# Performance work log

Hardware: AMD Instinct MI355X
Metric: run time of the kernel (lower is better)

The kernel has to match this reference:

```python
import jax, jax.numpy as jnp
import numpy as np

CAPACITY_FACTOR = 1.0


def setup_inputs() -> dict:
    key = jax.random.key(0)
    k = jax.random.split(key, 6)
    N, E, M, V = 8192, 8, 1024, 4096
    s = 0.02
    return {
        "x": jax.random.normal(k[0], (N, M), jnp.float32),
        "wg": jax.random.normal(k[1], (E, M), jnp.float32) * s,
        "fc1": jax.random.normal(k[2], (E, M, V), jnp.float32) * s,
        "b1": jax.random.normal(k[3], (E, V), jnp.float32) * s,
        "fc2": jax.random.normal(k[4], (E, V, M), jnp.float32) * s,
        "b2": jax.random.normal(k[5], (E, M), jnp.float32) * s,
    }


def reference(x, wg, fc1, b1, fc2, b2):
    N, M = x.shape
    E = wg.shape[0]
    capacity = 2 * int(CAPACITY_FACTOR * ((N + E - 1) // E))  # Top2 capacity

    # ---- Top2 gating ----
    logits = x @ wg.T                                   # [N, E]
    gates = jax.nn.softmax(logits, axis=1)
    _, top2 = jax.lax.top_k(logits, 2)                  # [N, 2]
    i1, i2 = top2[:, 0], top2[:, 1]
    m1 = jax.nn.one_hot(i1, E, dtype=jnp.int32)         # [N, E]
    m2 = jax.nn.one_hot(i2, E, dtype=jnp.int32)
    g1 = jnp.sum(gates * m1, axis=1)                    # [N]
    g2 = jnp.sum(gates * m2, axis=1)

    # cumulative-sum capacity assignment (per expert slot index)
    loc1 = jnp.cumsum(m1, axis=0) - 1                   # [N, E]
    loc2 = jnp.cumsum(m2, axis=0) - 1 + jnp.sum(m1, axis=0, keepdims=True)
    m1c = m1 * (loc1 < capacity).astype(jnp.int32)
    m2c = m2 * (loc2 < capacity).astype(jnp.int32)
    loc1_s = jnp.sum(loc1 * m1c, axis=1)                # [N]
    loc2_s = jnp.sum(loc2 * m2c, axis=1)
    v1 = jnp.sum(m1c, axis=1)                           # 0/1 kept flags
    v2 = jnp.sum(m2c, axis=1)

    # aux load-balancing loss (fp32 branch of original)
    me = jnp.sum(gates, axis=0)
    ce = jnp.sum(m1c.astype(gates.dtype), axis=0)
    l_aux = jnp.sum(me * ce) * (E / (N * N))

    # ---- dispatch (scatter tokens into [E*C, M]) ----
    idx1 = jnp.where(v1 > 0, i1 * capacity + loc1_s, -1)
    idx2 = jnp.where(v2 > 0, i2 * capacity + loc2_s, -1)
    disp = jnp.zeros((E * capacity, M), x.dtype)
    disp = disp.at[idx1].add(x, mode="drop")
    disp = disp.at[idx2].add(x, mode="drop")

    # ---- fused FFN experts ----
    d = disp.reshape(E, capacity, M)
    h = jnp.einsum("ecm,emv->ecv", d, fc1) + b1[:, None, :]
    h = jax.nn.relu(h)
    y = jnp.einsum("ecv,evm->ecm", h, fc2) + b2[:, None, :]
    yf = y.reshape(E * capacity, M)

    # ---- combine (gather + gate-weighted sum) ----
    v1f = v1.astype(x.dtype)
    v2f = v2.astype(x.dtype)
    out = (g1 * v1f)[:, None] * yf[i1 * capacity + loc1_s] \
        + (g2 * v2f)[:, None] * yf[i2 * capacity + loc2_s]
    return out, l_aux
```

## Files before the change

kernel.cpp:

```cpp
#include <hip/hip_runtime.h>
#include <stdint.h>

typedef __attribute__((ext_vector_type(8))) short short8;
typedef __attribute__((ext_vector_type(4))) float f32x4;

#define N_TOK 8192
#define E_EXP 8
#define M_DIM 1024
#define V_DIM 4096
#define CAP   2048
#define SLOTS (E_EXP*CAP)

__device__ __forceinline__ unsigned short f2bf(float f){
  unsigned u = __float_as_uint(f);
  u += 0x7FFFu + ((u >> 16) & 1u);
  return (unsigned short)(u >> 16);
}

__device__ __forceinline__ void gload_lds16(const void* g, void* l){
  __builtin_amdgcn_global_load_lds(
    (const __attribute__((address_space(1))) void*)g,
    (__attribute__((address_space(3))) void*)l, 16, 0, 0);
}

__global__ __launch_bounds__(256) void routing_kernel(
    const float* __restrict__ x, const float* __restrict__ wg,
    float* __restrict__ gates, int* __restrict__ i1o, int* __restrict__ i2o,
    float* __restrict__ g1o, float* __restrict__ g2o)
{
  int wv = threadIdx.x >> 6, lane = threadIdx.x & 63;
  int n = blockIdx.x * 4 + wv;
  const float* xr = x + (size_t)n * M_DIM;
  double acc[8];
  #pragma unroll
  for (int e = 0; e < 8; e++) acc[e] = 0.0;
  for (int j = 0; j < M_DIM/64; j++){
    double xv = (double)xr[lane + j*64];
    #pragma unroll
    for (int e = 0; e < 8; e++) acc[e] += xv * (double)wg[e*M_DIM + lane + j*64];
  }
  #pragma unroll
  for (int off = 32; off > 0; off >>= 1){
    #pragma unroll
    for (int e = 0; e < 8; e++) acc[e] += __shfl_down(acc[e], off);
  }
  if (lane == 0){
    float lg[8], mx = -1e30f;
    #pragma unroll
    for (int e = 0; e < 8; e++){ lg[e] = (float)acc[e]; mx = fmaxf(mx, lg[e]); }
    float s = 0.f, gt[8];
    #pragma unroll
    for (int e = 0; e < 8; e++){ gt[e] = expf(lg[e] - mx); s += gt[e]; }
    float inv = 1.f / s;
    int i1 = 0;
    #pragma unroll
    for (int e = 1; e < 8; e++) if (lg[e] > lg[i1]) i1 = e;
    int i2 = (i1 == 0) ? 1 : 0;
    #pragma unroll
    for (int e = 0; e < 8; e++){ if (e == i1) continue; if (lg[e] > lg[i2]) i2 = e; }
    #pragma unroll
    for (int e = 0; e < 8; e++) gates[(size_t)n*8 + e] = gt[e] * inv;
    i1o[n] = i1; i2o[n] = i2;
    g1o[n] = gt[i1] * inv; g2o[n] = gt[i2] * inv;
  }
}

__global__ __launch_bounds__(1024) void scan_kernel(
    const int* __restrict__ i1, const int* __restrict__ i2,
    int* __restrict__ s1, int* __restrict__ s2, int* __restrict__ ce_out)
{
  __shared__ unsigned long long sc[4][1024];
  const int t = threadIdx.x;
  int e1l[8], e2l[8];
  unsigned long long c[4] = {0ull,0ull,0ull,0ull};
  #pragma unroll
  for (int k = 0; k < 8; k++){
    int a = i1[t*8+k]; e1l[k] = a; c[a>>2]       += 1ull << ((a&3)*16);
    int b = i2[t*8+k]; e2l[k] = b; c[2 + (b>>2)] += 1ull << ((b&3)*16);
  }
  #pragma unroll
  for (int i = 0; i < 4; i++) sc[i][t] = c[i];
  __syncthreads();
  for (int st = 1; st < 1024; st <<= 1){
    unsigned long long add[4];
    #pragma unroll
    for (int i = 0; i < 4; i++) add[i] = (t >= st) ? sc[i][t-st] : 0ull;
    __syncthreads();
    #pragma unroll
    for (int i = 0; i < 4; i++) if (t >= st) sc[i][t] += add[i];
    __syncthreads();
  }
  unsigned long long ex[4], tot[4];
  #pragma unroll
  for (int i = 0; i < 4; i++){ ex[i] = sc[i][t] - c[i]; tot[i] = sc[i][1023]; }
  int r1[8], r2[8], t1[8];
  #pragma unroll
  for (int e = 0; e < 8; e++){
    r1[e] = (int)((ex[e>>2]       >> ((e&3)*16)) & 0xFFFF);
    r2[e] = (int)((ex[2 + (e>>2)] >> ((e&3)*16)) & 0xFFFF);
    t1[e] = (int)((tot[e>>2]      >> ((e&3)*16)) & 0xFFFF);
  }
  #pragma unroll
  for (int k = 0; k < 8; k++){
    int n = t*8 + k;
    int a = e1l[k]; int loc1 = r1[a]++;
    s1[n] = (loc1 < CAP) ? (a*CAP + loc1) : -1;
    int b = e2l[k]; int loc2 = r2[b]++ + t1[b];
    s2[n] = (loc2 < CAP) ? (b*CAP + loc2) : -1;
  }
  if (t == 0){
    #pragma unroll
    for (int e = 0; e < 8; e++) ce_out[e] = (t1[e] < CAP) ? t1[e] : CAP;
  }
}

__global__ __launch_bounds__(1024) void laux_kernel(
    const float* __restrict__ gates, const int* __restrict__ ce, float* __restrict__ dst)
{
  __shared__ float red[1024];
  const int t = threadIdx.x;
  float part[8];
  #pragma unroll
  for (int e = 0; e < 8; e++) part[e] = 0.f;
  for (int k = 0; k < 8; k++){
    int n = t + k*1024;
    #pragma unroll
    for (int e = 0; e < 8; e++) part[e] += gates[(size_t)n*8 + e];
  }
  float laux = 0.f;
  for (int e = 0; e < 8; e++){
    red[t] = part[e];
    __syncthreads();
    for (int s = 512; s > 0; s >>= 1){ if (t < s) red[t] += red[t+s]; __syncthreads(); }
    if (t == 0) laux += red[0] * (float)ce[e];
    __syncthreads();
  }
  if (t == 0) dst[0] = laux * (float)(8.0/(8192.0*8192.0));
}

__global__ void build_droplist(const int* __restrict__ s1, const int* __restrict__ s2,
                               int* __restrict__ list, int* __restrict__ cnt)
{
  int lane = threadIdx.x;
  int base = 0;
  int a = s1[lane], b = s2[lane];
  for (int it = 0; it < N_TOK/64; it++){
    int na = 0, nb = 0;
    if (it + 1 < N_TOK/64){
      na = s1[(it+1)*64 + lane];
      nb = s2[(it+1)*64 + lane];
    }
    int n = it*64 + lane;
    bool f1 = (a == -1) || (a == SLOTS-1);
    unsigned long long m1 = __ballot(f1);
    if (f1) list[base + __popcll(m1 & ((1ull<<lane)-1))] = n;
    base += __popcll(m1);
    bool f2 = (b == -1) || (b == SLOTS-1);
    unsigned long long m2 = __ballot(f2);
    if (f2) list[base + __popcll(m2 & ((1ull<<lane)-1))] = n;
    base += __popcll(m2);
    a = na; b = nb;
  }
  if (lane == 0) *cnt = base;
}

__global__ void dropacc1_kernel(const float* __restrict__ x, const int* __restrict__ list,
                                const int* __restrict__ cnt, float* __restrict__ partial)
{
  int col = blockIdx.x*256 + threadIdx.x;
  int sl  = blockIdx.y;
  int c = *cnt;
  int per = (c + 15) >> 4;
  int lo = sl*per, hi = lo + per; if (hi > c) hi = c;
  float a = 0.f;
  for (int i = lo; i < hi; i++) a += x[(size_t)list[i]*M_DIM + col];
  partial[sl*M_DIM + col] = a;
}
__global__ void dropacc2_kernel(const float* __restrict__ partial, float* __restrict__ drow)
{
  int col = blockIdx.x*256 + threadIdx.x;
  float s = 0.f;
  #pragma unroll
  for (int j = 0; j < 16; j++) s += partial[j*M_DIM + col];
  drow[col] = s;
}

template<bool RELU>
__global__ __launch_bounds__(256) void fix_gemv(
    const float* __restrict__ vec, const float* __restrict__ W,
    const float* __restrict__ bias, float* __restrict__ outv, int K, int N)
{
  __shared__ float red[256];
  const int o = threadIdx.x & 15;
  const int c = threadIdx.x >> 4;
  const int n = blockIdx.x*16 + o;
  const int chunk = K >> 4;
  float a = 0.f;
  for (int k = c*chunk; k < (c+1)*chunk; k++) a += vec[k] * W[(size_t)k*N + n];
  red[threadIdx.x] = a;
  __syncthreads();
  if (c == 0){
    float s = 0.f;
    #pragma unroll
    for (int j = 0; j < 16; j++) s += red[o + j*16];
    s += bias[n];
    if (RELU) s = fmaxf(s, 0.f);
    outv[n] = s;
  }
}

__global__ __launch_bounds__(256) void convert_x_kernel(
    const float* __restrict__ x, unsigned short* __restrict__ xb)
{
  size_t i = ((size_t)blockIdx.x*256 + threadIdx.x) * 8;
  float4 f0 = *(const float4*)(x + i);
  float4 f1 = *(const float4*)(x + i + 4);
  short8 v;
  v[0] = (short)f2bf(f0.x); v[1] = (short)f2bf(f0.y);
  v[2] = (short)f2bf(f0.z); v[3] = (short)f2bf(f0.w);
  v[4] = (short)f2bf(f1.x); v[5] = (short)f2bf(f1.y);
  v[6] = (short)f2bf(f1.z); v[7] = (short)f2bf(f1.w);
  *(short8*)(xb + i) = v;
}

__global__ void tok_fill_kernel(const int* __restrict__ s1, const int* __restrict__ s2,
                                int* __restrict__ tok)
{
  int n = blockIdx.x*256 + threadIdx.x;
  int a = s1[n], b = s2[n];
  if (a >= 0) tok[a] = n;
  if (b >= 0) tok[b] = n;
}

__global__ __launch_bounds__(256) void transpose_f32_bf16(
    const float* __restrict__ in, unsigned short* __restrict__ out,
    int R, int C, size_t estride)
{
  __shared__ float tile[32][33];
  const size_t eo = (size_t)blockIdx.z * estride;
  int c0 = blockIdx.x*32, r0 = blockIdx.y*32;
  int tx = threadIdx.x & 31, ty = threadIdx.x >> 5;
  #pragma unroll
  for (int j = 0; j < 4; j++)
    tile[ty + j*8][tx] = in[eo + (size_t)(r0 + ty + j*8)*C + (c0 + tx)];
  __syncthreads();
  #pragma unroll
  for (int j = 0; j < 4; j++)
    out[eo + (size_t)(c0 + ty + j*8)*R + (r0 + tx)] = f2bf(tile[tx][ty + j*8]);
}

template<bool RELU_BF16, bool AIND>
__global__ __launch_bounds__(512, 2) void gemm_tn(
    const unsigned short* __restrict__ A, size_t aE,
    const unsigned short* __restrict__ B, size_t bE,
    const float* __restrict__ bias, size_t biasE,
    void* __restrict__ outp, size_t oE, int K, int Ncols, int gx, int gy,
    const int* __restrict__ tok, const unsigned short* __restrict__ xb,
    const unsigned short* __restrict__ zrow, int slotbase)
{
  __shared__ unsigned short SH[65536];
  auto As = reinterpret_cast<unsigned short(*)[2][128*64]>(SH);
  auto Bs = reinterpret_cast<unsigned short(*)[2][128*64]>(SH + 32768);
  const int nwg = gridDim.x;
  const int orig = blockIdx.x;
  const int wgid = (orig & 7) * (nwg >> 3) + (orig >> 3);
  const int z  = wgid / (gx*gy);
  const int rr = wgid - z*gx*gy;
  const int by = rr / gx, bx = rr - by*gx;

  const unsigned short* Be = B + (size_t)z * bE;
  const float* be = bias + (size_t)z * biasE;
  const int row0 = by * 256;
  const int col0 = bx * 256;
  const int tid = threadIdx.x;
  const int lane = tid & 63, wv = tid >> 6;
  const int wr = wv >> 2, wc = wv & 3;
  const int frow = lane & 15, fq = lane >> 4;

  const int rbase = (wv*64 + lane) >> 3;
  const int swz   = (((lane & 7) ^ (rbase & 7)) * 8);
  const unsigned short* pA[2][2];
  const unsigned short* pB[2][2];
  #pragma unroll
  for (int h = 0; h < 2; h++)
    #pragma unroll
    for (int i = 0; i < 2; i++){
      int gr = row0 + h*128 + rbase + i*64;
      if (AIND){
        int tk = tok[slotbase + z*CAP + gr];
        pA[h][i] = (tk < 0) ? zrow : (xb + (size_t)tk * M_DIM);
      } else {
        pA[h][i] = A + (size_t)z * aE + (size_t)gr * K;
      }
      pB[h][i] = Be + (size_t)(col0 + h*128 + rbase + i*64) * K;
    }

  f32x4 acc[8][4];
  #pragma unroll
  for (int i = 0; i < 8; i++)
    #pragma unroll
    for (int j = 0; j < 4; j++) acc[i][j] = (f32x4){0.f,0.f,0.f,0.f};

  auto STAGE_A = [&](int buf, int half, int k0){
    #pragma unroll
    for (int i = 0; i < 2; i++)
      gload_lds16(pA[half][i] + k0 + swz, &As[buf][half][(i*512 + wv*64)*8]);
  };
  auto STAGE_B = [&](int buf, int half, int k0){
    #pragma unroll
    for (int i = 0; i < 2; i++)
      gload_lds16(pB[half][i] + k0 + swz, &Bs[buf][half][(i*512 + wv*64)*8]);
  };

  short8 a[8], bA[4], bB[4];
  auto READ_A = [&](int buf, int fmb){
    #pragma unroll
    for (int fm = 0; fm < 4; fm++)
      #pragma unroll
      for (int ks = 0; ks < 2; ks++){
        int row = wr*128 + (fmb+fm)*16 + frow;
        int h = row >> 7, r = row & 127;
        int sl = (ks*4 + fq) ^ (r & 7);
        a[fm*2+ks] = *(const short8*)&As[buf][h][r*64 + sl*8];
      }
  };
  auto READ_B = [&](int buf, int fnb, short8* dst){
    #pragma unroll
    for (int fn = 0; fn < 2; fn++)
      #pragma unroll
      for (int ks = 0; ks < 2; ks++){
        int col = wc*64 + (fnb+fn)*16 + frow;
        int h = col >> 7, r = col & 127;
        int sl = (ks*4 + fq) ^ (r & 7);
        dst[fn*2+ks] = *(const short8*)&Bs[buf][h][r*64 + sl*8];
      }
  };
  auto MFMA16 = [&](int fmb, int fnb, short8* b){
    #pragma unroll
    for (int fm = 0; fm < 4; fm++)
      #pragma unroll
      for (int fn = 0; fn < 2; fn++)
        #pragma unroll
        for (int ks = 0; ks < 2; ks++)
          acc[fmb+fm][fnb+fn] =
            __builtin_amdgcn_mfma_f32_16x16x32_bf16(a[fm*2+ks], b[fn*2+ks], acc[fmb+fm][fnb+fn], 0, 0, 0);
  };

  const int nt = K >> 6;
  const int iters = nt >> 1;
  STAGE_A(0, 0, 0); STAGE_A(0, 1, 0);
  STAGE_B(0, 0, 0); STAGE_B(0, 1, 0);
  STAGE_B(1, 0, 64); STAGE_B(1, 1, 64);
  asm volatile("s_waitcnt vmcnt(4)" ::: "memory");
  __builtin_amdgcn_sched_barrier(0);
  __builtin_amdgcn_s_barrier();

  for (int t = 0; t < iters; ++t){
    const bool more = (t + 1 < iters);
    const int kO = (2*t+1)*64;
    const int kN = (2*t+2)*64;
    const int kL = (2*t+3)*64;

    READ_A(0, 0); READ_B(0, 0, bA);
    STAGE_A(1, 0, kO);
    __builtin_amdgcn_s_barrier();
    asm volatile("s_waitcnt lgkmcnt(0)" ::: "memory");
    __builtin_amdgcn_sched_barrier(0);
    __builtin_amdgcn_s_setprio(1); MFMA16(0, 0, bA); __builtin_amdgcn_s_setprio(0);
    __builtin_amdgcn_s_barrier();
    READ_B(0, 2, bB);
    STAGE_A(1, 1, kO);
    __builtin_amdgcn_s_barrier();
    asm volatile("s_waitcnt lgkmcnt(0)" ::: "memory");
    __builtin_amdgcn_sched_barrier(0);
    __builtin_amdgcn_s_setprio(1); MFMA16(0, 2, bB); __builtin_amdgcn_s_setprio(0);
    __builtin_amdgcn_s_barrier();
    READ_A(0, 4);
    if (more) STAGE_B(0, 0, kN);
    __builtin_amdgcn_s_barrier();
    asm volatile("s_waitcnt lgkmcnt(0)" ::: "memory");
    __builtin_amdgcn_sched_barrier(0);
    __builtin_amdgcn_s_setprio(1); MFMA16(4, 0, bA); __builtin_amdgcn_s_setprio(0);
    __builtin_amdgcn_s_barrier();
    if (more) STAGE_B(0, 1, kN);
    __builtin_amdgcn_s_barrier();
    asm volatile("s_waitcnt lgkmcnt(0)" ::: "memory");
    __builtin_amdgcn_sched_barrier(0);
    __builtin_amdgcn_s_setprio(1); MFMA16(4, 2, bB); __builtin_amdgcn_s_setprio(0);
    if (more) asm volatile("s_waitcnt vmcnt(4)" ::: "memory");
    else      asm volatile("s_waitcnt vmcnt(0)" ::: "memory");
    __builtin_amdgcn_sched_barrier(0);
    __builtin_amdgcn_s_barrier();

    READ_A(1, 0); READ_B(1, 0, bA);
    if (more) STAGE_A(0, 0, kN);
    __builtin_amdgcn_s_barrier();
    asm volatile("s_waitcnt lgkmcnt(0)" ::: "memory");
    __builtin_amdgcn_sched_barrier(0);
    __builtin_amdgcn_s_setprio(1); MFMA16(0, 0, bA); __builtin_amdgcn_s_setprio(0);
    __builtin_amdgcn_s_barrier();
    READ_B(1, 2, bB);
    if (more) STAGE_A(0, 1, kN);
    __builtin_amdgcn_s_barrier();
    asm volatile("s_waitcnt lgkmcnt(0)" ::: "memory");
    __builtin_amdgcn_sched_barrier(0);
    __builtin_amdgcn_s_setprio(1); MFMA16(0, 2, bB); __builtin_amdgcn_s_setprio(0);
    __builtin_amdgcn_s_barrier();
    READ_A(1, 4);
    if (more) STAGE_B(1, 0, kL);
    __builtin_amdgcn_s_barrier();
    asm volatile("s_waitcnt lgkmcnt(0)" ::: "memory");
    __builtin_amdgcn_sched_barrier(0);
    __builtin_amdgcn_s_setprio(1); MFMA16(4, 0, bA); __builtin_amdgcn_s_setprio(0);
    __builtin_amdgcn_s_barrier();
    if (more) STAGE_B(1, 1, kL);
    __builtin_amdgcn_s_barrier();
    asm volatile("s_waitcnt lgkmcnt(0)" ::: "memory");
    __builtin_amdgcn_sched_barrier(0);
    __builtin_amdgcn_s_setprio(1); MFMA16(4, 2, bB); __builtin_amdgcn_s_setprio(0);
    if (more){
      asm volatile("s_waitcnt vmcnt(4)" ::: "memory");
      __builtin_amdgcn_sched_barrier(0);
    }
    __builtin_amdgcn_s_barrier();
  }

  const int rsub = fq * 4;
  if (RELU_BF16){
    unsigned short* ep = SH;
    #pragma unroll
    for (int fn = 0; fn < 4; fn++){
      int col = wc*64 + fn*16 + frow;
      float bv = be[col0 + col];
      #pragma unroll
      for (int fm = 0; fm < 8; fm++){
        int row = wr*128 + fm*16 + rsub;
        #pragma unroll
        for (int r = 0; r < 4; r++)
          ep[(row + r)*256 + col] = f2bf(fmaxf(acc[fm][fn][r] + bv, 0.f));
      }
    }
    __builtin_amdgcn_s_barrier();
    unsigned short* hp = (unsigned short*)outp + (size_t)z*oE;
    #pragma unroll
    for (int j = 0; j < 16; j++){
      int chunk = tid + j*512;
      int row = chunk >> 5, off = (chunk & 31)*8;
      *(short8*)(hp + (size_t)(row0 + row)*Ncols + col0 + off) = *(const short8*)&ep[row*256 + off];
    }
  } else {
    float* ep32 = (float*)SH;
    float* yp = (float*)outp + (size_t)z*oE;
    #pragma unroll
    for (int ph = 0; ph < 2; ph++){
      if (wr == ph){
        #pragma unroll
        for (int fn = 0; fn < 4; fn++){
          int col = wc*64 + fn*16 + frow;
          float bv = be[col0 + col];
          #pragma unroll
          for (int fm = 0; fm < 8; fm++){
            int rloc = fm*16 + rsub;
            #pragma unroll
            for (int r = 0; r < 4; r++)
              ep32[(rloc + r)*256 + col] = acc[fm][fn][r] + bv;
          }
        }
      }
      __builtin_amdgcn_s_barrier();
      #pragma unroll
      for (int j = 0; j < 16; j++){
        int chunk = tid + j*512;
        int rloc = chunk >> 6, off = (chunk & 63)*4;
        *(f32x4*)(yp + (size_t)(row0 + ph*128 + rloc)*Ncols + col0 + off) = *(const f32x4*)&ep32[rloc*256 + off];
      }
      __builtin_amdgcn_s_barrier();
    }
  }
}

__global__ void gather_full_kernel(const float* __restrict__ y, const int* __restrict__ s1,
    const int* __restrict__ s2, const float* __restrict__ g1, const float* __restrict__ g2,
    float* __restrict__ out)
{
  int n = blockIdx.x, t = threadIdx.x;
  int a = s1[n], b = s2[n];
  float c1 = (a >= 0) ? g1[n] : 0.f; int p1 = (a >= 0) ? a : 0;
  float c2 = (b >= 0) ? g2[n] : 0.f; int p2 = (b >= 0) ? b : 0;
  const float4 v1 = *(const float4*)(y + (size_t)p1*M_DIM + t*4);
  const float4 v2 = *(const float4*)(y + (size_t)p2*M_DIM + t*4);
  float4 o;
  o.x = c1*v1.x + c2*v2.x; o.y = c1*v1.y + c2*v2.y;
  o.z = c1*v1.z + c2*v2.z; o.w = c1*v1.w + c2*v2.w;
  *(float4*)(out + (size_t)n*M_DIM + t*4) = o;
}

__global__ void gather_kernel(const float* __restrict__ yB, const int* __restrict__ s1,
    const int* __restrict__ s2, const float* __restrict__ g1, const float* __restrict__ g2,
    float* __restrict__ out, int e0, int epb)
{
  int n = blockIdx.x, t = threadIdx.x;
  int a = s1[n], b = s2[n];
  float4 o;
  bool touched = false;
  for (int z = 0; z < epb; z++){
    int e = e0 + z;
    float coef = 0.f; int loc = 0; bool m = false;
    if (a >= 0 && (a >> 11) == e){ coef = g1[n]; loc = a & (CAP-1); m = true; }
    else if (b >= 0 && (b >> 11) == e){ coef = g2[n]; loc = b & (CAP-1); m = true; }
    if (m){
      if (!touched) o = *(const float4*)(out + (size_t)n*M_DIM + t*4);
      const float4 v = *(const float4*)(yB + ((size_t)z*CAP + loc)*M_DIM + t*4);
      o.x += coef*v.x; o.y += coef*v.y; o.z += coef*v.z; o.w += coef*v.w;
      touched = true;
    }
  }
  if (touched) *(float4*)(out + (size_t)n*M_DIM + t*4) = o;
}

extern "C" void kernel_launch(void* const* d_in, const int* in_sizes, int n_in,
                              void* d_out, int out_size, void* d_ws, size_t ws_size,
                              hipStream_t stream)
{
  const float* x   = (const float*)d_in[0];
  const float* wg  = (const float*)d_in[1];
  const float* fc1 = (const float*)d_in[2];
  const float* b1  = (const float*)d_in[3];
  const float* fc2 = (const float*)d_in[4];
  const float* b2  = (const float*)d_in[5];
  float* out = (float*)d_out;
  char* ws = (char*)d_ws;

  size_t off = 0;
  auto take = [&](size_t b)->char*{ char* p = ws + off; off += (b + 255) & ~(size_t)255; return p; };

  float* gates = (float*)take((size_t)N_TOK*8*4);
  int*   i1    = (int*)  take((size_t)N_TOK*4);
  int*   i2    = (int*)  take((size_t)N_TOK*4);
  float* g1    = (float*)take((size_t)N_TOK*4);
  float* g2    = (float*)take((size_t)N_TOK*4);
  int*   s1    = (int*)  take((size_t)N_TOK*4);
  int*   s2    = (int*)  take((size_t)N_TOK*4);
  int*   ce    = (int*)  take(256);
  int*   list  = (int*)  take((size_t)2*N_TOK*4);
  int*   cnt   = (int*)  take(256);
  float* dpart = (float*)take((size_t)16*M_DIM*4);
  float* drow  = (float*)take((size_t)M_DIM*4);
  float* hrow  = (float*)take((size_t)V_DIM*4);
  unsigned short* xb   = (unsigned short*)take((size_t)N_TOK*M_DIM*2);
  int*            tok  = (int*)           take((size_t)SLOTS*4);
  unsigned short* zrow = (unsigned short*)take((size_t)M_DIM*2);

  const size_t perExp = (size_t)M_DIM*V_DIM*2*2
                      + (size_t)CAP*V_DIM*2
                      + (size_t)CAP*M_DIM*4;
  int epb = 0;
  {
    const int cands[3] = {8, 4, 2};
    for (int ci = 0; ci < 3; ci++){
      if (off + (size_t)cands[ci]*perExp + (1u<<20) <= ws_size){ epb = cands[ci]; break; }
    }
  }
  if (!epb){
    hipMemsetAsync(d_out, 0, (size_t)out_size*4, stream);
    return;
  }
  unsigned short* fc1bB = (unsigned short*)take((size_t)epb*M_DIM*V_DIM*2);
  unsigned short* fc2bB = (unsigned short*)take((size_t)epb*M_DIM*V_DIM*2);
  unsigned short* hB    = (unsigned short*)take((size_t)epb*CAP*V_DIM*2);
  float*          yB    = (float*)         take((size_t)epb*CAP*M_DIM*4);

  routing_kernel<<<N_TOK/4, 256, 0, stream>>>(x, wg, gates, i1, i2, g1, g2);
  scan_kernel<<<1, 1024, 0, stream>>>(i1, i2, s1, s2, ce);
  laux_kernel<<<1, 1024, 0, stream>>>(gates, ce, out + (size_t)N_TOK*M_DIM);
  if (epb < 8) hipMemsetAsync(out, 0, (size_t)N_TOK*M_DIM*4, stream);
  hipMemsetAsync(tok, 0xFF, (size_t)SLOTS*4, stream);
  hipMemsetAsync(zrow, 0, (size_t)M_DIM*2, stream);
  tok_fill_kernel<<<N_TOK/256, 256, 0, stream>>>(s1, s2, tok);
  convert_x_kernel<<<(N_TOK*M_DIM)/(256*8), 256, 0, stream>>>(x, xb);
  build_droplist<<<1, 64, 0, stream>>>(s1, s2, list, cnt);
  dropacc1_kernel<<<dim3(4,16), 256, 0, stream>>>(x, list, cnt, dpart);
  dropacc2_kernel<<<4, 256, 0, stream>>>(dpart, drow);

  const size_t eW = (size_t)M_DIM*V_DIM;
  for (int e0 = 0; e0 < E_EXP; e0 += epb){
    transpose_f32_bf16<<<dim3(V_DIM/32, M_DIM/32, epb), 256, 0, stream>>>(fc1 + (size_t)e0*eW, fc1bB, M_DIM, V_DIM, eW);
    transpose_f32_bf16<<<dim3(M_DIM/32, V_DIM/32, epb), 256, 0, stream>>>(fc2 + (size_t)e0*eW, fc2bB, V_DIM, M_DIM, eW);
    gemm_tn<true, true><<<(V_DIM/256)*(CAP/256)*epb, 512, 0, stream>>>(
        nullptr, 0, fc1bB, eW, b1 + (size_t)e0*V_DIM, V_DIM,
        hB, (size_t)CAP*V_DIM, M_DIM, V_DIM, V_DIM/256, CAP/256,
        tok, xb, zrow, e0*CAP);
    gemm_tn<false, false><<<(M_DIM/256)*(CAP/256)*epb, 512, 0, stream>>>(
        hB, (size_t)CAP*V_DIM, fc2bB, eW, b2 + (size_t)e0*M_DIM, M_DIM,
        yB, (size_t)CAP*M_DIM, V_DIM, M_DIM, M_DIM/256, CAP/256,
        nullptr, nullptr, nullptr, 0);
    if (E_EXP-1 >= e0 && E_EXP-1 < e0+epb){
      fix_gemv<true ><<<V_DIM/16, 256, 0, stream>>>(drow, fc1 + (size_t)(E_EXP-1)*eW, b1 + (size_t)(E_EXP-1)*V_DIM, hrow, M_DIM, V_DIM);
      fix_gemv<false><<<M_DIM/16, 256, 0, stream>>>(hrow, fc2 + (size_t)(E_EXP-1)*eW, b2 + (size_t)(E_EXP-1)*M_DIM,
                                                    yB + ((size_t)(E_EXP-1-e0)*CAP + (CAP-1))*M_DIM, V_DIM, M_DIM);
    }
    if (epb < 8)
      gather_kernel<<<N_TOK, 256, 0, stream>>>(yB, s1, s2, g1, g2, out, e0, epb);
  }
  if (epb == 8)
    gather_full_kernel<<<N_TOK, 256, 0, stream>>>(yB, s1, s2, g1, g2, out);
}
```

Before: 591.1 us.

## Fold routing bookkeeping into scan kernel and merge conversion/transpose launches

Merges the laux reduction, the tok fill and memset, the zrow clear and the drop-list build into the single-block scan kernel, replacing several small launches and memsets. When all experts fit in the workspace, one prep kernel now does the x bf16 conversion and both weight transposes. The aim is to cut launch overhead and serialized tiny kernels. In exchange, more serial work now runs inside a single 1024-thread block, and the drop list is ordered per thread instead of per token pass.

Result: faster. 558.2 us (-5.6%).

```diff
diff --git a/kernel.cpp b/kernel.cpp
--- a/kernel.cpp
+++ b/kernel.cpp
@@ -67,10 +67,18 @@
 
 __global__ __launch_bounds__(1024) void scan_kernel(
     const int* __restrict__ i1, const int* __restrict__ i2,
-    int* __restrict__ s1, int* __restrict__ s2, int* __restrict__ ce_out)
+    const float* __restrict__ gates,
+    int* __restrict__ s1, int* __restrict__ s2,
+    int* __restrict__ tok, unsigned short* __restrict__ zrow,
+    int* __restrict__ list, int* __restrict__ cnt,
+    float* __restrict__ laux_dst)
 {
   __shared__ unsigned long long sc[4][1024];
   const int t = threadIdx.x;
+  #pragma unroll
+  for (int i = 0; i < SLOTS/1024; i++) tok[t + i*1024] = -1;
+  if (t < 512) ((unsigned int*)zrow)[t] = 0u;
+
   int e1l[8], e2l[8];
   unsigned long long c[4] = {0ull,0ull,0ull,0ull};
   #pragma unroll
@@ -100,68 +108,62 @@
     r2[e] = (int)((ex[2 + (e>>2)] >> ((e&3)*16)) & 0xFFFF);
     t1[e] = (int)((tot[e>>2]      >> ((e&3)*16)) & 0xFFFF);
   }
+  unsigned int dmask = 0;
   #pragma unroll
   for (int k = 0; k < 8; k++){
     int n = t*8 + k;
     int a = e1l[k]; int loc1 = r1[a]++;
-    s1[n] = (loc1 < CAP) ? (a*CAP + loc1) : -1;
+    int v1 = (loc1 < CAP) ? (a*CAP + loc1) : -1;
+    s1[n] = v1;
+    if (v1 >= 0) tok[v1] = n;
+    if (v1 == -1 || v1 == SLOTS-1) dmask |= (1u << (2*k));
     int b = e2l[k]; int loc2 = r2[b]++ + t1[b];
-    s2[n] = (loc2 < CAP) ? (b*CAP + loc2) : -1;
-  }
-  if (t == 0){
-    #pragma unroll
-    for (int e = 0; e < 8; e++) ce_out[e] = (t1[e] < CAP) ? t1[e] : CAP;
-  }
-}
-
-__global__ __launch_bounds__(1024) void laux_kernel(
-    const float* __restrict__ gates, const int* __restrict__ ce, float* __restrict__ dst)
-{
-  __shared__ float red[1024];
-  const int t = threadIdx.x;
+    int v2 = (loc2 < CAP) ? (b*CAP + loc2) : -1;
+    s2[n] = v2;
+    if (v2 >= 0) tok[v2] = n;
+    if (v2 == -1 || v2 == SLOTS-1) dmask |= (1u << (2*k+1));
+  }
+  unsigned int* pc = (unsigned int*)&sc[0][0];
+  int myc = __popc(dmask);
+  __syncthreads();
+  pc[t] = (unsigned)myc;
+  __syncthreads();
+  for (int st = 1; st < 1024; st <<= 1){
+    unsigned int v = (t >= st) ? pc[t - st] : 0u;
+    __syncthreads();
+    pc[t] += v;
+    __syncthreads();
+  }
+  int pre = (int)pc[t] - myc;
+  if (t == 1023) *cnt = (int)pc[1023];
+  #pragma unroll
+  for (int k = 0; k < 8; k++){
+    if (dmask & (1u << (2*k)))   list[pre++] = t*8 + k;
+    if (dmask & (1u << (2*k+1))) list[pre++] = t*8 + k;
+  }
   float part[8];
   #pragma unroll
   for (int e = 0; e < 8; e++) part[e] = 0.f;
+  #pragma unroll
   for (int k = 0; k < 8; k++){
-    int n = t + k*1024;
+    int n = t*8 + k;
     #pragma unroll
     for (int e = 0; e < 8; e++) part[e] += gates[(size_t)n*8 + e];
   }
+  float* red = (float*)&sc[2][0];
   float laux = 0.f;
+  __syncthreads();
   for (int e = 0; e < 8; e++){
     red[t] = part[e];
     __syncthreads();
     for (int s = 512; s > 0; s >>= 1){ if (t < s) red[t] += red[t+s]; __syncthreads(); }
-    if (t == 0) laux += red[0] * (float)ce[e];
+    if (t == 0){
+      int cee = (t1[e] < CAP) ? t1[e] : CAP;
+      laux += red[0] * (float)cee;
+    }
     __syncthreads();
   }
-  if (t == 0) dst[0] = laux * (float)(8.0/(8192.0*8192.0));
-}
-
-__global__ void build_droplist(const int* __restrict__ s1, const int* __restrict__ s2,
-                               int* __restrict__ list, int* __restrict__ cnt)
-{
-  int lane = threadIdx.x;
-  int base = 0;
-  int a = s1[lane], b = s2[lane];
-  for (int it = 0; it < N_TOK/64; it++){
-    int na = 0, nb = 0;
-    if (it + 1 < N_TOK/64){
-      na = s1[(it+1)*64 + lane];
-      nb = s2[(it+1)*64 + lane];
-    }
-    int n = it*64 + lane;
-    bool f1 = (a == -1) || (a == SLOTS-1);
-    unsigned long long m1 = __ballot(f1);
-    if (f1) list[base + __popcll(m1 & ((1ull<<lane)-1))] = n;
-    base += __popcll(m1);
-    bool f2 = (b == -1) || (b == SLOTS-1);
-    unsigned long long m2 = __ballot(f2);
-    if (f2) list[base + __popcll(m2 & ((1ull<<lane)-1))] = n;
-    base += __popcll(m2);
-    a = na; b = nb;
-  }
-  if (lane == 0) *cnt = base;
+  if (t == 0) laux_dst[0] = laux * (float)(8.0/(8192.0*8192.0));
 }
 
 __global__ void dropacc1_kernel(const float* __restrict__ x, const int* __restrict__ list,
@@ -223,15 +225,6 @@
   *(short8*)(xb + i) = v;
 }
 
-__global__ void tok_fill_kernel(const int* __restrict__ s1, const int* __restrict__ s2,
-                                int* __restrict__ tok)
-{
-  int n = blockIdx.x*256 + threadIdx.x;
-  int a = s1[n], b = s2[n];
-  if (a >= 0) tok[a] = n;
-  if (b >= 0) tok[b] = n;
-}
-
 __global__ __launch_bounds__(256) void transpose_f32_bf16(
     const float* __restrict__ in, unsigned short* __restrict__ out,
     int R, int C, size_t estride)
@@ -247,6 +240,44 @@
   #pragma unroll
   for (int j = 0; j < 4; j++)
     out[eo + (size_t)(c0 + ty + j*8)*R + (r0 + tx)] = f2bf(tile[tx][ty + j*8]);
+}
+
+__global__ __launch_bounds__(256) void prep_kernel(
+    const float* __restrict__ x, unsigned short* __restrict__ xb,
+    const float* __restrict__ fc1, unsigned short* __restrict__ fc1b,
+    const float* __restrict__ fc2, unsigned short* __restrict__ fc2b)
+{
+  __shared__ float tile[32][33];
+  int bid = blockIdx.x;
+  if (bid < 4096){
+    size_t i = ((size_t)bid*256 + threadIdx.x) * 8;
+    float4 f0 = *(const float4*)(x + i);
+    float4 f1 = *(const float4*)(x + i + 4);
+    short8 v;
+    v[0] = (short)f2bf(f0.x); v[1] = (short)f2bf(f0.y);
+    v[2] = (short)f2bf(f0.z); v[3] = (short)f2bf(f0.w);
+    v[4] = (short)f2bf(f1.x); v[5] = (short)f2bf(f1.y);
+    v[6] = (short)f2bf(f1.z); v[7] = (short)f2bf(f1.w);
+    *(short8*)(xb + i) = v;
+    return;
+  }
+  bid -= 4096;
+  const int mat = bid >> 15;
+  const int rem = bid & 32767;
+  const int e   = rem >> 12;
+  const int tl  = rem & 4095;
+  const size_t eo = (size_t)e * M_DIM * V_DIM;
+  const float* in; unsigned short* out; int R, C, c0, r0;
+  if (mat == 0){ in = fc1 + eo; out = fc1b + eo; R = M_DIM; C = V_DIM; c0 = (tl & 127)*32; r0 = (tl >> 7)*32; }
+  else         { in = fc2 + eo; out = fc2b + eo; R = V_DIM; C = M_DIM; c0 = (tl & 31)*32;  r0 = (tl >> 5)*32; }
+  int tx = threadIdx.x & 31, ty = threadIdx.x >> 5;
+  #pragma unroll
+  for (int j = 0; j < 4; j++)
+    tile[ty + j*8][tx] = in[(size_t)(r0 + ty + j*8)*C + (c0 + tx)];
+  __syncthreads();
+  #pragma unroll
+  for (int j = 0; j < 4; j++)
+    out[(size_t)(c0 + ty + j*8)*R + (r0 + tx)] = f2bf(tile[tx][ty + j*8]);
 }
 
 template<bool RELU_BF16, bool AIND>
@@ -541,7 +572,6 @@
   float* g2    = (float*)take((size_t)N_TOK*4);
   int*   s1    = (int*)  take((size_t)N_TOK*4);
   int*   s2    = (int*)  take((size_t)N_TOK*4);
-  int*   ce    = (int*)  take(256);
   int*   list  = (int*)  take((size_t)2*N_TOK*4);
   int*   cnt   = (int*)  take(256);
   float* dpart = (float*)take((size_t)16*M_DIM*4);
@@ -571,21 +601,23 @@
   float*          yB    = (float*)         take((size_t)epb*CAP*M_DIM*4);
 
   routing_kernel<<<N_TOK/4, 256, 0, stream>>>(x, wg, gates, i1, i2, g1, g2);
-  scan_kernel<<<1, 1024, 0, stream>>>(i1, i2, s1, s2, ce);
-  laux_kernel<<<1, 1024, 0, stream>>>(gates, ce, out + (size_t)N_TOK*M_DIM);
-  if (epb < 8) hipMemsetAsync(out, 0, (size_t)N_TOK*M_DIM*4, stream);
-  hipMemsetAsync(tok, 0xFF, (size_t)SLOTS*4, stream);
-  hipMemsetAsync(zrow, 0, (size_t)M_DIM*2, stream);
-  tok_fill_kernel<<<N_TOK/256, 256, 0, stream>>>(s1, s2, tok);
-  convert_x_kernel<<<(N_TOK*M_DIM)/(256*8), 256, 0, stream>>>(x, xb);
-  build_droplist<<<1, 64, 0, stream>>>(s1, s2, list, cnt);
+  scan_kernel<<<1, 1024, 0, stream>>>(i1, i2, gates, s1, s2, tok, zrow, list, cnt,
+                                      out + (size_t)N_TOK*M_DIM);
+  if (epb == 8){
+    prep_kernel<<<4096 + 65536, 256, 0, stream>>>(x, xb, fc1, fc1bB, fc2, fc2bB);
+  } else {
+    hipMemsetAsync(out, 0, (size_t)N_TOK*M_DIM*4, stream);
+    convert_x_kernel<<<(N_TOK*M_DIM)/(256*8), 256, 0, stream>>>(x, xb);
+  }
   dropacc1_kernel<<<dim3(4,16), 256, 0, stream>>>(x, list, cnt, dpart);
   dropacc2_kernel<<<4, 256, 0, stream>>>(dpart, drow);
 
   const size_t eW = (size_t)M_DIM*V_DIM;
   for (int e0 = 0; e0 < E_EXP; e0 += epb){
-    transpose_f32_bf16<<<dim3(V_DIM/32, M_DIM/32, epb), 256, 0, stream>>>(fc1 + (size_t)e0*eW, fc1bB, M_DIM, V_DIM, eW);
-    transpose_f32_bf16<<<dim3(M_DIM/32, V_DIM/32, epb), 256, 0, stream>>>(fc2 + (size_t)e0*eW, fc2bB, V_DIM, M_DIM, eW);
+    if (epb < 8){
+      transpose_f32_bf16<<<dim3(V_DIM/32, M_DIM/32, epb), 256, 0, stream>>>(fc1 + (size_t)e0*eW, fc1bB, M_DIM, V_DIM, eW);
+      transpose_f32_bf16<<<dim3(M_DIM/32, V_DIM/32, epb), 256, 0, stream>>>(fc2 + (size_t)e0*eW, fc2bB, V_DIM, M_DIM, eW);
+    }
     gemm_tn<true, true><<<(V_DIM/256)*(CAP/256)*epb, 512, 0, stream>>>(
         nullptr, 0, fc1bB, eW, b1 + (size_t)e0*V_DIM, V_DIM,
         hB, (size_t)CAP*V_DIM, M_DIM, V_DIM, V_DIM/256, CAP/256,
```
